# Optimization experiments

Measured on AMD Instinct MI355X. Metric: run time of the kernel, lower is better.

The kernel has to match this reference:

```python
import jax, jax.numpy as jnp
import numpy as np

D_MODEL = 1024
NUM_HEADS = 16
D_K = D_MODEL // NUM_HEADS  # 64
THETA = 10000.0
MAX_SEQ_LEN = 2048


def _trunc_normal(key, shape, std):
    # approximate trunc_normal_(mean=0, std, a=-3*std, b=3*std)
    u = jax.random.truncated_normal(key, -3.0, 3.0, shape, dtype=jnp.float32)
    return u * std


def setup_inputs() -> dict:
    key = jax.random.key(0)
    ks = jax.random.split(key, 5)
    x = jax.random.normal(ks[0], (2, 2048, D_MODEL), dtype=jnp.float32)
    token_positions = jnp.arange(2048, dtype=jnp.int64 if jax.config.jax_enable_x64 else jnp.int32)
    sigma = 2.0 / (D_MODEL + D_MODEL)
    Wq = _trunc_normal(ks[1], (D_MODEL, D_MODEL), sigma)
    Wk = _trunc_normal(ks[2], (D_MODEL, D_MODEL), sigma)
    Wv = _trunc_normal(ks[3], (D_MODEL, D_MODEL), sigma)
    Wo = _trunc_normal(ks[4], (D_MODEL, D_MODEL), sigma)
    return {"in_features": x, "Wq": Wq, "Wk": Wk, "Wv": Wv, "Wo": Wo,
            "token_positions": token_positions}


def _rope(x, cos_phi, sin_phi):
    # x: (..., seq, d_k); cos/sin: (seq, d_k//2)
    x_even = x[..., 0::2]
    x_odd = x[..., 1::2]
    y_even = x_even * cos_phi - x_odd * sin_phi
    y_odd = x_even * sin_phi + x_odd * cos_phi
    # interleave back
    y = jnp.stack([y_even, y_odd], axis=-1)
    return y.reshape(x.shape)


def reference(in_features, Wq, Wk, Wv, Wo, token_positions):
    b, s, d = in_features.shape
    h, dk = NUM_HEADS, D_K
    # projections: weight is (d_out, d_in)
    q = jnp.einsum('bsd,ed->bse', in_features, Wq)
    k = jnp.einsum('bsd,ed->bse', in_features, Wk)
    v = jnp.einsum('bsd,ed->bse', in_features, Wv)
    # split heads: (b, h, s, dk)
    q = q.reshape(b, s, h, dk).transpose(0, 2, 1, 3)
    k = k.reshape(b, s, h, dk).transpose(0, 2, 1, 3)
    v = v.reshape(b, s, h, dk).transpose(0, 2, 1, 3)
    # RoPE tables
    inv_freq = 1.0 / (THETA ** (jnp.arange(0, dk, 2, dtype=jnp.float32) / dk))
    phi = token_positions.astype(jnp.float32)[:, None] * inv_freq[None, :]  # (s, dk/2)
    cos_phi, sin_phi = jnp.cos(phi), jnp.sin(phi)
    q = _rope(q, cos_phi, sin_phi)
    k = _rope(k, cos_phi, sin_phi)
    # causal mask
    mask = jnp.tril(jnp.ones((s, s), dtype=bool))
    scores = jnp.einsum('bhqd,bhkd->bhqk', q, k) / jnp.sqrt(jnp.float32(dk))
    scores = jnp.where(mask, scores, -jnp.inf)
    attn = jax.nn.softmax(scores, axis=-1)
    out = jnp.einsum('bhqk,bhkd->bhqd', attn, v)
    out = out.transpose(0, 2, 1, 3).reshape(b, s, d)
    return jnp.einsum('bsd,ed->bse', out, Wo)
```

## Files before the change

kernel.cpp:

```cpp
#include <hip/hip_runtime.h>
#include <hip/hip_bf16.h>
#include <math.h>

#define S_  2048
#define DM_ 1024

typedef unsigned short u16;
typedef __attribute__((ext_vector_type(8))) short short8;
typedef __attribute__((ext_vector_type(4))) float f32x4;

__device__ __forceinline__ u16 f2bf(float f) {
  unsigned u = __float_as_uint(f);
  u += 0x7fffu + ((u >> 16) & 1u);
  return (u16)(u >> 16);
}
__device__ __forceinline__ float bf2f(u16 h) {
  return __uint_as_float((unsigned)h << 16);
}
__device__ __forceinline__ unsigned pack_bf2(float a, float b) {
  union { __hip_bfloat162 h2; unsigned u; } cv;
  cv.h2 = __float22bfloat162_rn(float2{a, b});
  return cv.u;
}
__device__ __forceinline__ void cp16(const void* g, void* l) {
  __builtin_amdgcn_global_load_lds(
      (const __attribute__((address_space(1))) unsigned*)(uintptr_t)g,
      (__attribute__((address_space(3))) unsigned*)(unsigned)(uintptr_t)l, 16, 0, 0);
}

struct CastArgs { const float* src[5]; u16* dst[5]; int n[5]; };

__global__ __launch_bounds__(256) void cast_kernel(CastArgs a) {
  const int z = blockIdx.y;
  const int i = (blockIdx.x * 256 + threadIdx.x) * 8;
  if (i >= a.n[z]) return;
  const float4* s = (const float4*)(a.src[z] + i);
  float4 v0 = s[0], v1 = s[1];
  short8 r;
  r[0] = (short)f2bf(v0.x); r[1] = (short)f2bf(v0.y);
  r[2] = (short)f2bf(v0.z); r[3] = (short)f2bf(v0.w);
  r[4] = (short)f2bf(v1.x); r[5] = (short)f2bf(v1.y);
  r[6] = (short)f2bf(v1.z); r[7] = (short)f2bf(v1.w);
  *(short8*)(a.dst[z] + i) = r;
}

struct GemmArgs { const u16* A; const u16* W[3]; void* out[3]; int modes; };

__global__ __launch_bounds__(256) void gemm_mfma(GemmArgs g) {
  __shared__ __align__(16) u16 As[2][4096];
  __shared__ __align__(16) u16 Bs[2][4096];
  const int tid = threadIdx.x, lane = tid & 63, w = tid >> 6;
  const int wr = w >> 1, wc = w & 1;
  const int z = blockIdx.z;
  const u16* __restrict__ A = g.A;
  const u16* __restrict__ W = g.W[z];
  const int m0 = blockIdx.y * 128, n0 = blockIdx.x * 128;

  const f32x4 fzero = {0.f, 0.f, 0.f, 0.f};
  f32x4 acc[4][4];
  #pragma unroll
  for (int i = 0; i < 4; i++)
    #pragma unroll
    for (int j = 0; j < 4; j++) acc[i][j] = fzero;

  const int c0 = tid >> 7;
  const int rs = tid & 127;
  const int fq = (lane >> 4) * 2048;
  const int fr = (lane & 15) * 16;

  const u16* Arow = A + (size_t)(m0 + rs) * 1024;
  const u16* Wrow = W + (size_t)(n0 + rs) * 1024;

  cp16(Arow + c0 * 8,       (char*)As[0] + w * 1024);
  cp16(Arow + (c0 + 2) * 8, (char*)As[0] + 4096 + w * 1024);
  cp16(Wrow + c0 * 8,       (char*)Bs[0] + w * 1024);
  cp16(Wrow + (c0 + 2) * 8, (char*)Bs[0] + 4096 + w * 1024);
  __syncthreads();

  for (int kt = 0; kt < 32; kt++) {
    const int cur = kt & 1, nxt = cur ^ 1;
    if (kt < 31) {
      const int k1 = (kt + 1) * 32;
      cp16(Arow + k1 + c0 * 8,       (char*)As[nxt] + w * 1024);
      cp16(Arow + k1 + (c0 + 2) * 8, (char*)As[nxt] + 4096 + w * 1024);
      cp16(Wrow + k1 + c0 * 8,       (char*)Bs[nxt] + w * 1024);
      cp16(Wrow + k1 + (c0 + 2) * 8, (char*)Bs[nxt] + 4096 + w * 1024);
    }

    short8 af[4], bf_[4];
    #pragma unroll
    for (int mt = 0; mt < 4; mt++)
      af[mt] = *(const short8*)((const char*)As[cur] + fq + (wr * 64 + mt * 16) * 16 + fr);
    #pragma unroll
    for (int nt = 0; nt < 4; nt++)
      bf_[nt] = *(const short8*)((const char*)Bs[cur] + fq + (wc * 64 + nt * 16) * 16 + fr);
    #pragma unroll
    for (int mt = 0; mt < 4; mt++)
      #pragma unroll
      for (int nt = 0; nt < 4; nt++)
        acc[mt][nt] = __builtin_amdgcn_mfma_f32_16x16x32_bf16(af[mt], bf_[nt], acc[mt][nt], 0, 0, 0);
    __syncthreads();
  }

  const int mode = (g.modes >> (2 * z)) & 3;
  const int rbase = m0 + wr * 64 + (lane >> 4) * 4;
  const int cbase = n0 + wc * 64 + (lane & 15);
  if (mode == 0) {
    u16* O = (u16*)g.out[z];
    #pragma unroll
    for (int mt = 0; mt < 4; mt++)
      #pragma unroll
      for (int nt = 0; nt < 4; nt++)
        #pragma unroll
        for (int r = 0; r < 4; r++)
          O[(size_t)(rbase + mt * 16 + r) * 1024 + cbase + nt * 16] = f2bf(acc[mt][nt][r]);
  } else if (mode == 1) {
    u16* O = (u16*)g.out[z];
    #pragma unroll
    for (int mt = 0; mt < 4; mt++)
      #pragma unroll
      for (int nt = 0; nt < 4; nt++) {
        int gr = rbase + mt * 16;
        int b = gr >> 11, s0 = gr & (S_ - 1);
        int gc = cbase + nt * 16;
        int h = gc >> 6, d = gc & 63;
        ushort4 v;
        v.x = f2bf(acc[mt][nt][0]); v.y = f2bf(acc[mt][nt][1]);
        v.z = f2bf(acc[mt][nt][2]); v.w = f2bf(acc[mt][nt][3]);
        *(ushort4*)&O[(size_t)((b * 16 + h) * 64 + d) * 2048 + s0] = v;
      }
  } else {
    float* O = (float*)g.out[z];
    #pragma unroll
    for (int mt = 0; mt < 4; mt++)
      #pragma unroll
      for (int nt = 0; nt < 4; nt++)
        #pragma unroll
        for (int r = 0; r < 4; r++)
          O[(size_t)(rbase + mt * 16 + r) * 1024 + cbase + nt * 16] = acc[mt][nt][r];
  }
}

__global__ __launch_bounds__(256) void rope_kernel(u16* qb, u16* kb, const int* __restrict__ tp) {
  const int isq = (blockIdx.y == 0);
  u16* p = isq ? qb : kb;
  const float outscale = isq ? 0.18033688011112042f : 1.0f;
  const int i = (blockIdx.x * 256 + threadIdx.x) * 8;
  const int s = (i >> 10) & (S_ - 1);
  const int d = i & 63;
  const float pos = (float)tp[s];
  short8 v = *(short8*)(p + i);
  #pragma unroll
  for (int j = 0; j < 4; j++) {
    float inv = exp2f(-(float)(d + 2 * j) * 0.20762050593046439f);
    float phi = pos * inv;
    float sn, cs;
    sincosf(phi, &sn, &cs);
    float xe = bf2f((u16)v[2 * j]), xo = bf2f((u16)v[2 * j + 1]);
    v[2 * j]     = (short)f2bf((xe * cs - xo * sn) * outscale);
    v[2 * j + 1] = (short)f2bf((xe * sn + xo * cs) * outscale);
  }
  *(short8*)(p + i) = v;
}

__global__ __launch_bounds__(512, 4) void attn_mfma(const u16* __restrict__ qb, const u16* __restrict__ kb,
                                                    const u16* __restrict__ vt, u16* __restrict__ ab) {
  __shared__ __align__(16) u16 Qs[2][4096];
  __shared__ __align__(16) u16 Ks[2][4096];
  __shared__ __align__(16) u16 Vs[2][4096];

  const int tid = threadIdx.x, lane = tid & 63, w = tid >> 6;
  const int v = w & 3, g = w >> 2;
  const int t = lane & 15, u = lane >> 4;
  const int bh = blockIdx.y, b = bh >> 4, h = bh & 15;
  const int i = blockIdx.x;
  const int qa = 31 - i;
  const int qbt = i;
  const int nk = 32 - i;
  const size_t qkb = (size_t)b * S_ * 1024 + h * 64;
  const size_t vtb = (size_t)bh * 64 * 2048;

  {
    const int qtile = g ? qbt : qa;
    cp16(qb + qkb + (size_t)(qtile * 64 + lane) * 1024 + v * 8,       (char*)Qs[g] + v * 1024);
    cp16(qb + qkb + (size_t)(qtile * 64 + lane) * 1024 + (v + 4) * 8, (char*)Qs[g] + 4096 + v * 1024);
  }
  cp16(kb + qkb + (size_t)lane * 1024 + w * 8, (char*)Ks[0] + w * 1024);
  cp16(vt + vtb + (size_t)lane * 2048 + w * 8, (char*)Vs[0] + w * 1024);
  __syncthreads();

  short8 aqA[2], aqP[2];
  #pragma unroll
  for (int ks = 0; ks < 2; ks++) {
    aqA[ks] = *(const short8*)((const char*)Qs[0] + (ks * 4 + u) * 1024 + (v * 16 + t) * 16);
    short8 bq = *(const short8*)((const char*)Qs[1] + (ks * 4 + u) * 1024 + (v * 16 + t) * 16);
    aqP[ks] = g ? bq : aqA[ks];
  }

  const f32x4 fzero = {0.f, 0.f, 0.f, 0.f};
  f32x4 oPrim[4], oSec[4];
  #pragma unroll
  for (int ct = 0; ct < 4; ct++) { oPrim[ct] = fzero; oSec[ct] = fzero; }
  float rsumP = 0.f, rsumS = 0.f;

  const int qprim = g ? qbt : qa;
  const int qrowP = qprim * 64 + v * 16 + t;
  const int qrowA = qa * 64 + v * 16 + t;

  for (int kt = 0; kt < nk; kt++) {
    const int cur = kt & 1, nxt = cur ^ 1;
    if (kt + 1 < nk) {
      cp16(kb + qkb + (size_t)((kt + 1) * 64 + lane) * 1024 + w * 8, (char*)Ks[nxt] + w * 1024);
      cp16(vt + vtb + (size_t)lane * 2048 + (kt + 1) * 64 + w * 8,   (char*)Vs[nxt] + w * 1024);
    }

    if (kt <= qbt) {
      f32x4 st[4] = {fzero, fzero, fzero, fzero};
      #pragma unroll
      for (int ks = 0; ks < 2; ks++)
        #pragma unroll
        for (int ct = 0; ct < 4; ct++) {
          short8 kf = *(const short8*)((const char*)Ks[cur] + (ks * 4 + u) * 1024 + (ct * 16 + t) * 16);
          st[ct] = __builtin_amdgcn_mfma_f32_16x16x32_bf16(kf, aqP[ks], st[ct], 0, 0, 0);
        }

      unsigned pb2[4][2];
      const bool diag = (kt == qprim);
      #pragma unroll
      for (int ct = 0; ct < 4; ct++) {
        float p[4];
        #pragma unroll
        for (int r = 0; r < 4; r++) {
          int key = kt * 64 + ct * 16 + 4 * u + r;
          float pv = exp2f(st[ct][r]);
          p[r] = (diag && key > qrowP) ? 0.f : pv;
          rsumP += p[r];
        }
        pb2[ct][0] = pack_bf2(p[0], p[1]);
        pb2[ct][1] = pack_bf2(p[2], p[3]);
      }

      #pragma unroll
      for (int ks = 0; ks < 2; ks++) {
        union { short8 s8; int i4[4]; } pf;
        #pragma unroll
        for (int jj = 0; jj < 4; jj++) {
          int src = 32 * (u & 1) + 16 * (jj >> 1) + t;
          int v0 = __shfl((int)pb2[ks * 2][jj & 1], src, 64);
          int v1 = __shfl((int)pb2[ks * 2 + 1][jj & 1], src, 64);
          pf.i4[jj] = (u >> 1) ? v1 : v0;
        }
        #pragma unroll
        for (int ct = 0; ct < 4; ct++) {
          short8 vf = *(const short8*)((const char*)Vs[cur] + (ks * 4 + u) * 1024 + (ct * 16 + t) * 16);
          oPrim[ct] = __builtin_amdgcn_mfma_f32_16x16x32_bf16(vf, pf.s8, oPrim[ct], 0, 0, 0);
        }
      }
    } else {
      f32x4 st2[2] = {fzero, fzero};
      #pragma unroll
      for (int ks = 0; ks < 2; ks++)
        #pragma unroll
        for (int c = 0; c < 2; c++) {
          short8 kf = *(const short8*)((const char*)Ks[cur] + (ks * 4 + u) * 1024 + ((2 * g + c) * 16 + t) * 16);
          st2[c] = __builtin_amdgcn_mfma_f32_16x16x32_bf16(kf, aqA[ks], st2[c], 0, 0, 0);
        }

      unsigned ph[2][2];
      float rs = 0.f;
      const bool diag = (kt == qa);
      #pragma unroll
      for (int c = 0; c < 2; c++) {
        float p[4];
        #pragma unroll
        for (int r = 0; r < 4; r++) {
          int key = kt * 64 + (2 * g + c) * 16 + 4 * u + r;
          float pv = exp2f(st2[c][r]);
          p[r] = (diag && key > qrowA) ? 0.f : pv;
          rs += p[r];
        }
        ph[c][0] = pack_bf2(p[0], p[1]);
        ph[c][1] = pack_bf2(p[2], p[3]);
      }

      union { short8 s8; int i4[4]; } pf;
      #pragma unroll
      for (int jj = 0; jj < 4; jj++) {
        int src = 32 * (u & 1) + 16 * (jj >> 1) + t;
        int v0 = __shfl((int)ph[0][jj & 1], src, 64);
        int v1 = __shfl((int)ph[1][jj & 1], src, 64);
        pf.i4[jj] = (u >> 1) ? v1 : v0;
      }
      if (g) {
        rsumS += rs;
        #pragma unroll
        for (int ct = 0; ct < 4; ct++) {
          short8 vf = *(const short8*)((const char*)Vs[cur] + (4 + u) * 1024 + (ct * 16 + t) * 16);
          oSec[ct] = __builtin_amdgcn_mfma_f32_16x16x32_bf16(vf, pf.s8, oSec[ct], 0, 0, 0);
        }
      } else {
        rsumP += rs;
        #pragma unroll
        for (int ct = 0; ct < 4; ct++) {
          short8 vf = *(const short8*)((const char*)Vs[cur] + u * 1024 + (ct * 16 + t) * 16);
          oPrim[ct] = __builtin_amdgcn_mfma_f32_16x16x32_bf16(vf, pf.s8, oPrim[ct], 0, 0, 0);
        }
      }
    }
    __syncthreads();
  }

  float* dmpO = (float*)Ks;
  float* dmpR = (float*)Vs;
  if (g) {
    #pragma unroll
    for (int ct = 0; ct < 4; ct++)
      *(f32x4*)&dmpO[(size_t)(v * 64 + lane) * 16 + ct * 4] = oSec[ct];
    dmpR[v * 64 + lane] = rsumS;
    float rs = rsumP;
    rs += __shfl_xor(rs, 16, 64);
    rs += __shfl_xor(rs, 32, 64);
    const float inv = 1.0f / rs;
    #pragma unroll
    for (int ct = 0; ct < 4; ct++) {
      ushort4 vv;
      vv.x = f2bf(oPrim[ct][0] * inv); vv.y = f2bf(oPrim[ct][1] * inv);
      vv.z = f2bf(oPrim[ct][2] * inv); vv.w = f2bf(oPrim[ct][3] * inv);
      *(ushort4*)&ab[((size_t)b * S_ + qrowP) * 1024 + h * 64 + ct * 16 + 4 * u] = vv;
    }
  }
  __syncthreads();
  if (!g) {
    #pragma unroll
    for (int ct = 0; ct < 4; ct++) {
      f32x4 add = *(const f32x4*)&dmpO[(size_t)(v * 64 + lane) * 16 + ct * 4];
      oPrim[ct] += add;
    }
    float rs = rsumP + dmpR[v * 64 + lane];
    rs += __shfl_xor(rs, 16, 64);
    rs += __shfl_xor(rs, 32, 64);
    const float inv = 1.0f / rs;
    #pragma unroll
    for (int ct = 0; ct < 4; ct++) {
      ushort4 vv;
      vv.x = f2bf(oPrim[ct][0] * inv); vv.y = f2bf(oPrim[ct][1] * inv);
      vv.z = f2bf(oPrim[ct][2] * inv); vv.w = f2bf(oPrim[ct][3] * inv);
      *(ushort4*)&ab[((size_t)b * S_ + qrowA) * 1024 + h * 64 + ct * 16 + 4 * u] = vv;
    }
  }
}

extern "C" void kernel_launch(void* const* d_in, const int* in_sizes, int n_in,
                              void* d_out, int out_size, void* d_ws, size_t ws_size,
                              hipStream_t stream) {
  const float* x  = (const float*)d_in[0];
  const float* Wq = (const float*)d_in[1];
  const float* Wk = (const float*)d_in[2];
  const float* Wv = (const float*)d_in[3];
  const float* Wo = (const float*)d_in[4];
  const int*   tp = (const int*)d_in[5];
  float* out = (float*)d_out;

  char* ws = (char*)d_ws;
  u16* xb  = (u16*)(ws);
  u16* wqb = (u16*)(ws + (8 << 20));
  u16* wkb = (u16*)(ws + (10 << 20));
  u16* wvb = (u16*)(ws + (12 << 20));
  u16* wob = (u16*)(ws + (14 << 20));
  u16* qbuf = (u16*)(ws + (16 << 20));
  u16* kbuf = (u16*)(ws + (24 << 20));
  u16* vtb  = (u16*)(ws + (32 << 20));
  u16* abuf = (u16*)(ws + (40 << 20));

  CastArgs ca;
  ca.src[0] = x;  ca.dst[0] = xb;  ca.n[0] = 2 * S_ * DM_;
  ca.src[1] = Wq; ca.dst[1] = wqb; ca.n[1] = DM_ * DM_;
  ca.src[2] = Wk; ca.dst[2] = wkb; ca.n[2] = DM_ * DM_;
  ca.src[3] = Wv; ca.dst[3] = wvb; ca.n[3] = DM_ * DM_;
  ca.src[4] = Wo; ca.dst[4] = wob; ca.n[4] = DM_ * DM_;
  cast_kernel<<<dim3(2048, 5), 256, 0, stream>>>(ca);

  GemmArgs gq;
  gq.A = xb;
  gq.W[0] = wqb; gq.W[1] = wkb; gq.W[2] = wvb;
  gq.out[0] = qbuf; gq.out[1] = kbuf; gq.out[2] = vtb;
  gq.modes = (1 << 4);
  gemm_mfma<<<dim3(8, 32, 3), 256, 0, stream>>>(gq);

  rope_kernel<<<dim3(2048, 2), 256, 0, stream>>>(qbuf, kbuf, tp);

  attn_mfma<<<dim3(16, 32), 512, 0, stream>>>(qbuf, kbuf, vtb, abuf);

  GemmArgs go;
  go.A = abuf;
  go.W[0] = wob; go.W[1] = wob; go.W[2] = wob;
  go.out[0] = out; go.out[1] = out; go.out[2] = out;
  go.modes = 2;
  gemm_mfma<<<dim3(8, 32, 1), 256, 0, stream>>>(go);
}
```

Measured before the change: 226.9 us.

## Rework bf16 GEMM into 256x128 tiles with triple-buffered swizzled LDS pipeline

```diff
diff --git a/kernel.cpp b/kernel.cpp
--- a/kernel.cpp
+++ b/kernel.cpp
@@ -46,65 +46,87 @@
 
 struct GemmArgs { const u16* A; const u16* W[3]; void* out[3]; int modes; };
 
-__global__ __launch_bounds__(256) void gemm_mfma(GemmArgs g) {
-  __shared__ __align__(16) u16 As[2][4096];
-  __shared__ __align__(16) u16 Bs[2][4096];
+#define SLOT_BYTES 49152
+#define NKT 16
+
+__global__ __launch_bounds__(512, 2) void gemm_mfma(GemmArgs g) {
+  __shared__ __align__(16) char lds[3 * SLOT_BYTES];
   const int tid = threadIdx.x, lane = tid & 63, w = tid >> 6;
-  const int wr = w >> 1, wc = w & 1;
+  const int wm = w >> 1, wn = w & 1;
+  const int t = lane & 15, u = lane >> 4;
+  const int l3 = lane >> 3, l7 = lane & 7;
   const int z = blockIdx.z;
+  const int m0 = blockIdx.y * 256, n0 = blockIdx.x * 128;
   const u16* __restrict__ A = g.A;
   const u16* __restrict__ W = g.W[z];
-  const int m0 = blockIdx.y * 128, n0 = blockIdx.x * 128;
-
-  const f32x4 fzero = {0.f, 0.f, 0.f, 0.f};
+
+  const int axor = l7 << 4;
+  const int ksw = (l7 ^ l3) * 8;
+  const u16* Ab = A + (size_t)(m0 + w * 8 + l3) * 1024 + ksw;
+  const u16* Wb = W + (size_t)(n0 + w * 8 + l3) * 1024 + ksw;
+  char* const ldsw = lds + w * 1024;
+
+  auto stg = [&](int kt, int slot, int r0, int r1) {
+    char* sb = ldsw + slot * SLOT_BYTES;
+    #pragma unroll
+    for (int r = r0; r <= r1; r++) {
+      if (r < 4) cp16(Ab + (size_t)r * 65536 + kt * 64, sb + r * 8192);
+      else       cp16(Wb + (size_t)(r - 4) * 65536 + kt * 64, sb + 32768 + (r - 4) * 8192);
+    }
+  };
+
+  const f32x4 fz = {0.f, 0.f, 0.f, 0.f};
   f32x4 acc[4][4];
   #pragma unroll
   for (int i = 0; i < 4; i++)
     #pragma unroll
-    for (int j = 0; j < 4; j++) acc[i][j] = fzero;
-
-  const int c0 = tid >> 7;
-  const int rs = tid & 127;
-  const int fq = (lane >> 4) * 2048;
-  const int fr = (lane & 15) * 16;
-
-  const u16* Arow = A + (size_t)(m0 + rs) * 1024;
-  const u16* Wrow = W + (size_t)(n0 + rs) * 1024;
-
-  cp16(Arow + c0 * 8,       (char*)As[0] + w * 1024);
-  cp16(Arow + (c0 + 2) * 8, (char*)As[0] + 4096 + w * 1024);
-  cp16(Wrow + c0 * 8,       (char*)Bs[0] + w * 1024);
-  cp16(Wrow + (c0 + 2) * 8, (char*)Bs[0] + 4096 + w * 1024);
-  __syncthreads();
-
-  for (int kt = 0; kt < 32; kt++) {
-    const int cur = kt & 1, nxt = cur ^ 1;
-    if (kt < 31) {
-      const int k1 = (kt + 1) * 32;
-      cp16(Arow + k1 + c0 * 8,       (char*)As[nxt] + w * 1024);
-      cp16(Arow + k1 + (c0 + 2) * 8, (char*)As[nxt] + 4096 + w * 1024);
-      cp16(Wrow + k1 + c0 * 8,       (char*)Bs[nxt] + w * 1024);
-      cp16(Wrow + k1 + (c0 + 2) * 8, (char*)Bs[nxt] + 4096 + w * 1024);
-    }
-
-    short8 af[4], bf_[4];
-    #pragma unroll
-    for (int mt = 0; mt < 4; mt++)
-      af[mt] = *(const short8*)((const char*)As[cur] + fq + (wr * 64 + mt * 16) * 16 + fr);
-    #pragma unroll
-    for (int nt = 0; nt < 4; nt++)
-      bf_[nt] = *(const short8*)((const char*)Bs[cur] + fq + (wc * 64 + nt * 16) * 16 + fr);
-    #pragma unroll
-    for (int mt = 0; mt < 4; mt++)
-      #pragma unroll
-      for (int nt = 0; nt < 4; nt++)
-        acc[mt][nt] = __builtin_amdgcn_mfma_f32_16x16x32_bf16(af[mt], bf_[nt], acc[mt][nt], 0, 0, 0);
-    __syncthreads();
+    for (int j = 0; j < 4; j++) acc[i][j] = fz;
+
+  stg(0, 0, 0, 5);
+  stg(1, 1, 0, 5);
+  asm volatile("s_waitcnt vmcnt(6)" ::: "memory");
+  __builtin_amdgcn_s_barrier();
+
+  int sc = 0;
+  for (int kt = 0; kt < NKT; kt++) {
+    const char* cs = lds + sc * SLOT_BYTES;
+    int sp = sc + 2; if (sp >= 3) sp -= 3;
+    const bool pf = (kt + 2 < NKT);
+
+    #pragma unroll
+    for (int ks = 0; ks < 2; ks++) {
+      short8 af[4], bfr[4];
+      const int co = (ks * 64 + u * 16) ^ axor;
+      const char* ap = cs + (wm * 64 + t) * 128 + co;
+      const char* bp = cs + 32768 + (wn * 64 + t) * 128 + co;
+      #pragma unroll
+      for (int mf = 0; mf < 4; mf++) af[mf] = *(const short8*)(ap + mf * 2048);
+      #pragma unroll
+      for (int nf = 0; nf < 4; nf++) bfr[nf] = *(const short8*)(bp + nf * 2048);
+      if (pf) stg(kt + 2, sp, ks * 3, ks * 3 + 2);
+
+      __builtin_amdgcn_s_barrier();
+      asm volatile("s_waitcnt lgkmcnt(0)" ::: "memory");
+      __builtin_amdgcn_sched_barrier(0);
+      __builtin_amdgcn_s_setprio(1);
+      #pragma unroll
+      for (int mf = 0; mf < 4; mf++)
+        #pragma unroll
+        for (int nf = 0; nf < 4; nf++)
+          acc[mf][nf] = __builtin_amdgcn_mfma_f32_16x16x32_bf16(af[mf], bfr[nf], acc[mf][nf], 0, 0, 0);
+      __builtin_amdgcn_s_setprio(0);
+      if (ks == 1) {
+        if (pf)                { asm volatile("s_waitcnt vmcnt(6)" ::: "memory"); }
+        else if (kt + 1 < NKT) { asm volatile("s_waitcnt vmcnt(0)" ::: "memory"); }
+      }
+      __builtin_amdgcn_s_barrier();
+    }
+    sc++; if (sc == 3) sc = 0;
   }
 
   const int mode = (g.modes >> (2 * z)) & 3;
-  const int rbase = m0 + wr * 64 + (lane >> 4) * 4;
-  const int cbase = n0 + wc * 64 + (lane & 15);
+  const int rbase = m0 + wm * 64 + u * 4;
+  const int cbase = n0 + wn * 64 + t;
   if (mode == 0) {
     u16* O = (u16*)g.out[z];
     #pragma unroll
@@ -385,7 +407,7 @@
   gq.W[0] = wqb; gq.W[1] = wkb; gq.W[2] = wvb;
   gq.out[0] = qbuf; gq.out[1] = kbuf; gq.out[2] = vtb;
   gq.modes = (1 << 4);
-  gemm_mfma<<<dim3(8, 32, 3), 256, 0, stream>>>(gq);
+  gemm_mfma<<<dim3(8, 16, 3), 512, 0, stream>>>(gq);
 
   rope_kernel<<<dim3(2048, 2), 256, 0, stream>>>(qbuf, kbuf, tp);
 
@@ -396,5 +418,5 @@
   go.W[0] = wob; go.W[1] = wob; go.W[2] = wob;
   go.out[0] = out; go.out[1] = out; go.out[2] = out;
   go.modes = 2;
-  gemm_mfma<<<dim3(8, 32, 1), 256, 0, stream>>>(go);
-}
+  gemm_mfma<<<dim3(8, 16, 1), 512, 0, stream>>>(go);
+}
```

Result: faster. 197.6 us (-12.9%).
